# Optimization experiments

Hardware: AMD Instinct MI355X
Metric: run time of the kernel (lower is better)

Reference implementation:

```python
import jax, jax.numpy as jnp
import numpy as np

N, E, D, H, G, OUT = 50000, 800000, 128, 128, 64, 10


def setup_inputs() -> dict:
    key = jax.random.key(0)
    ks = jax.random.split(key, 10)
    x = jax.random.normal(ks[0], (N, D), dtype=jnp.float32)
    edge_index = jax.random.randint(ks[1], (2, E), 0, N, dtype=jnp.int64)
    batch = jnp.sort(jax.random.randint(ks[2], (N,), 0, G, dtype=jnp.int64))
    s = 1.0 / np.sqrt(D)
    W0 = jax.random.normal(ks[3], (D, H), dtype=jnp.float32) * s
    W1 = jax.random.normal(ks[4], (H, H), dtype=jnp.float32) * s
    W2 = jax.random.normal(ks[5], (H, H), dtype=jnp.float32) * s
    M0w = jax.random.normal(ks[6], (H, H), dtype=jnp.float32) * s
    M0b = jnp.zeros((H,), dtype=jnp.float32)
    M1w = jax.random.normal(ks[7], (H, OUT), dtype=jnp.float32) * s
    M1b = jnp.zeros((OUT,), dtype=jnp.float32)
    return dict(x=x, W0=W0, W1=W1, W2=W2, M0w=M0w, M0b=M0b, M1w=M1w, M1b=M1b,
                edge_index=edge_index, batch=batch)


def gcn_conv(x, W, src, dst):
    # PyG GCNConv (bias=False): h = x @ W; out = D^-1/2 (A + I) D^-1/2 h
    h = x @ W
    deg = jnp.zeros((N,), h.dtype).at[dst].add(1.0) + 1.0  # +1 for self-loop
    dinv = deg ** -0.5
    w = dinv[src] * dinv[dst]  # [E]
    agg = jax.ops.segment_sum(h[src] * w[:, None], dst, num_segments=N)
    return agg + h * (dinv * dinv)[:, None]  # self-loop term


def reference(x, W0, W1, W2, M0w, M0b, M1w, M1b, edge_index, batch):
    src, dst = edge_index[0], edge_index[1]
    h = gcn_conv(x, W0, src, dst)
    h = gcn_conv(jax.nn.relu(h), W1, src, dst)
    h = gcn_conv(jax.nn.relu(h), W2, src, dst)
    # global mean pool over graphs
    sums = jax.ops.segment_sum(h, batch, num_segments=G)
    cnts = jax.ops.segment_sum(jnp.ones((N,), h.dtype), batch, num_segments=G)
    pooled = sums / jnp.maximum(cnts, 1.0)[:, None]
    out = pooled @ M0w + M0b
    out = jax.nn.relu(out) @ M1w + M1b
    return out
```

## Files before the change

### kernel.cpp

```cpp
#include <hip/hip_runtime.h>
#include <hip/hip_fp16.h>

#define NN 50000
#define NE 800000
#define DIM 128
#define NG 64
#define NOUT 10

#define NBKT 391
#define HBLK 256
#define CHUNK ((NE + HBLK - 1) / HBLK)
#define PSLICE 8

typedef __attribute__((ext_vector_type(8))) short short8;
typedef __attribute__((ext_vector_type(4))) float float4v;

__device__ __forceinline__ void bf16_split(float v, short& hi, short& lo) {
    unsigned u = __float_as_uint(v);
    unsigned hb = (u + 0x7FFFu + ((u >> 16) & 1u)) & 0xFFFF0000u;
    float res = v - __uint_as_float(hb);
    unsigned u2 = __float_as_uint(res);
    unsigned lb = (u2 + 0x7FFFu + ((u2 >> 16) & 1u)) >> 16;
    hi = (short)(hb >> 16);
    lo = (short)lb;
}

#define PREP_XB 48
#define PREP_HB (PREP_XB + NN * DIM / 2048)
#define PREP_NB (PREP_HB + HBLK + 1)
__global__ __launch_bounds__(256) void prep_kernel(const float* __restrict__ W0,
                                                   const float* __restrict__ W1,
                                                   const float* __restrict__ W2,
                                                   short* __restrict__ wsp,
                                                   const float* __restrict__ X,
                                                   short* __restrict__ Ahi,
                                                   short* __restrict__ Alo,
                                                   const int* __restrict__ ei,
                                                   int* __restrict__ blkhist,
                                                   const int* __restrict__ batch,
                                                   int* __restrict__ first) {
    __shared__ int h[NBKT];
    int bx = blockIdx.x;
    if (bx < PREP_XB) {
        int w = bx >> 4;
        int sub = bx & 15;
        const float* W = (w == 0) ? W0 : (w == 1) ? W1 : W2;
        short* Wh = wsp + w * 2 * DIM * DIM;
        short* Wl = Wh + DIM * DIM;
        #pragma unroll
        for (int t = 0; t < 4; ++t) {
            int idx = sub * 1024 + t * 256 + threadIdx.x;
            int k = idx >> 7, n = idx & 127;
            short hi, lo;
            bf16_split(W[idx], hi, lo);
            Wh[n * DIM + k] = hi;
            Wl[n * DIM + k] = lo;
        }
    } else if (bx < PREP_HB) {
        size_t base = (size_t)(bx - PREP_XB) * 2048;
        #pragma unroll
        for (int c = 0; c < 2; ++c) {
            size_t idx = base + c * 1024 + threadIdx.x * 4;
            float4 v = *(const float4*)(X + idx);
            short h0, l0, h1, l1, h2, l2, h3, l3;
            bf16_split(v.x, h0, l0);
            bf16_split(v.y, h1, l1);
            bf16_split(v.z, h2, l2);
            bf16_split(v.w, h3, l3);
            *(ushort4*)(Ahi + idx) = make_ushort4((unsigned short)h0, (unsigned short)h1,
                                                  (unsigned short)h2, (unsigned short)h3);
            *(ushort4*)(Alo + idx) = make_ushort4((unsigned short)l0, (unsigned short)l1,
                                                  (unsigned short)l2, (unsigned short)l3);
        }
    } else if (bx < PREP_NB - 1) {
        int b = bx - PREP_HB;
        for (int i = threadIdx.x; i < NBKT; i += 256) h[i] = 0;
        __syncthreads();
        int lo = b * CHUNK, hi = min(lo + CHUNK, NE);
        for (int e = lo + threadIdx.x; e < hi; e += 256)
            atomicAdd(&h[ei[NE + e] >> 7], 1);
        __syncthreads();
        for (int i = threadIdx.x; i < NBKT; i += 256)
            blkhist[b * NBKT + i] = h[i];
    } else {
        int g = threadIdx.x;
        if (g <= NG) {
            int lo = 0, hi = NN;
            while (lo < hi) {
                int mid = (lo + hi) >> 1;
                if (batch[mid] < g) lo = mid + 1; else hi = mid;
            }
            first[g] = lo;
        }
    }
}

__global__ __launch_bounds__(256) void scan_all(int* __restrict__ blkhist,
                                                int* __restrict__ bintot) {
    __shared__ int s[256];
    int bin = blockIdx.x;
    int t = threadIdx.x;
    int v = blkhist[t * NBKT + bin];
    s[t] = v;
    __syncthreads();
    #pragma unroll
    for (int off = 1; off < 256; off <<= 1) {
        int tv = (t >= off) ? s[t - off] : 0;
        __syncthreads();
        s[t] += tv;
        __syncthreads();
    }
    blkhist[t * NBKT + bin] = s[t] - v;
    if (t == 255) bintot[bin] = s[255];
}

__global__ __launch_bounds__(512) void base_scan_kernel(const int* __restrict__ bintot,
                                                        int* __restrict__ bucket_base) {
    __shared__ int s[512];
    int t = threadIdx.x;
    int v = (t < NBKT) ? bintot[t] : 0;
    s[t] = v;
    __syncthreads();
    #pragma unroll
    for (int off = 1; off < 512; off <<= 1) {
        int tv = (t >= off) ? s[t - off] : 0;
        __syncthreads();
        s[t] += tv;
        __syncthreads();
    }
    if (t <= NBKT) bucket_base[t] = s[t] - v;
}

__global__ __launch_bounds__(256) void bucket_scatter(const int* __restrict__ ei,
                                                      const int* __restrict__ blkhist,
                                                      const int* __restrict__ bucket_base,
                                                      unsigned* __restrict__ ebuf) {
    __shared__ int cur[NBKT];
    int b = blockIdx.x;
    for (int i = threadIdx.x; i < NBKT; i += 256)
        cur[i] = blkhist[b * NBKT + i] + bucket_base[i];
    __syncthreads();
    int lo = b * CHUNK, hi = min(lo + CHUNK, NE);
    for (int e = lo + threadIdx.x; e < hi; e += 256) {
        int s = ei[e];
        int d = ei[NE + e];
        int pos = atomicAdd(&cur[d >> 7], 1);
        ebuf[pos] = ((unsigned)(d & 127) << 16) | (unsigned)s;
    }
}

__global__ __launch_bounds__(128) void build_csr(const unsigned* __restrict__ ebuf,
                                                 const int* __restrict__ bucket_base,
                                                 int* __restrict__ rowoff,
                                                 int* __restrict__ csr_src,
                                                 float* __restrict__ dinv) {
    __shared__ int deg[128];
    __shared__ int loff[128];
    int g = blockIdx.x;
    int lo = bucket_base[g], hi = bucket_base[g + 1];
    int t = threadIdx.x;
    deg[t] = 0;
    __syncthreads();
    for (int p = lo + t; p < hi; p += 128)
        atomicAdd(&deg[ebuf[p] >> 16], 1);
    __syncthreads();
    int v = deg[t];
    loff[t] = v;
    __syncthreads();
    #pragma unroll
    for (int off = 1; off < 128; off <<= 1) {
        int tv = (t >= off) ? loff[t - off] : 0;
        __syncthreads();
        loff[t] += tv;
        __syncthreads();
    }
    int excl = loff[t] - v;
    int node = g * 128 + t;
    if (node < NN) {
        rowoff[node] = lo + excl;
        dinv[node] = 1.0f / sqrtf((float)v + 1.0f);
    }
    if (node == 0) rowoff[NN] = NE;
    deg[t] = lo + excl;
    __syncthreads();
    for (int p = lo + t; p < hi; p += 128) {
        unsigned pk = ebuf[p];
        int pos = atomicAdd(&deg[pk >> 16], 1);
        csr_src[pos] = (int)(pk & 0xFFFFu);
    }
}

#define WPAD 136
__global__ __launch_bounds__(256) void gemm_mfma(const short* __restrict__ Ahi,
                                                 const short* __restrict__ Alo,
                                                 const short* __restrict__ Wsp,
                                                 __half* __restrict__ Y, int nrows) {
    __shared__ short Wh[DIM * WPAD];
    __shared__ short Wl[DIM * WPAD];
    int tid = threadIdx.x;
    {
        const short8* gh = (const short8*)Wsp;
        const short8* gl = (const short8*)(Wsp + DIM * DIM);
        #pragma unroll
        for (int i = 0; i < 8; ++i) {
            int e = tid + 256 * i;
            int n = e >> 4;
            int k = (e & 15) * 8;
            *(short8*)&Wh[n * WPAD + k] = gh[e];
            *(short8*)&Wl[n * WPAD + k] = gl[e];
        }
    }
    int wave = tid >> 6;
    int lane = tid & 63;
    int lm = lane & 15;
    int lq = lane >> 4;
    int row_t0 = blockIdx.x * 128 + wave * 32;

    float4v acc[2][8];
    #pragma unroll
    for (int t = 0; t < 2; ++t)
        #pragma unroll
        for (int i = 0; i < 8; ++i) acc[t][i] = (float4v){0.f, 0.f, 0.f, 0.f};

    __syncthreads();
    #pragma unroll
    for (int kk = 0; kk < 4; ++kk) {
        short8 ah[2], al[2];
        #pragma unroll
        for (int t = 0; t < 2; ++t) {
            int r = min(row_t0 + t * 16 + lm, nrows - 1);
            size_t ao = (size_t)r * DIM + kk * 32 + lq * 8;
            ah[t] = *(const short8*)(Ahi + ao);
            al[t] = *(const short8*)(Alo + ao);
        }
        #pragma unroll
        for (int n0 = 0; n0 < 8; ++n0) {
            short8 bh = *(const short8*)&Wh[(n0 * 16 + lm) * WPAD + kk * 32 + lq * 8];
            short8 bl = *(const short8*)&Wl[(n0 * 16 + lm) * WPAD + kk * 32 + lq * 8];
            #pragma unroll
            for (int t = 0; t < 2; ++t) {
                acc[t][n0] = __builtin_amdgcn_mfma_f32_16x16x32_bf16(ah[t], bh, acc[t][n0], 0, 0, 0);
                acc[t][n0] = __builtin_amdgcn_mfma_f32_16x16x32_bf16(al[t], bh, acc[t][n0], 0, 0, 0);
                acc[t][n0] = __builtin_amdgcn_mfma_f32_16x16x32_bf16(ah[t], bl, acc[t][n0], 0, 0, 0);
            }
        }
    }
    #pragma unroll
    for (int t = 0; t < 2; ++t)
        #pragma unroll
        for (int n0 = 0; n0 < 8; ++n0)
            #pragma unroll
            for (int rg = 0; rg < 4; ++rg) {
                int row = row_t0 + t * 16 + lq * 4 + rg;
                if (row < nrows) Y[(size_t)row * DIM + n0 * 16 + lm] = __float2half(acc[t][n0][rg]);
            }
}

template <bool SPLIT>
__global__ __launch_bounds__(128) void agg_kernel(const __half* __restrict__ H,
                                                  __half* __restrict__ O16,
                                                  short* __restrict__ Ohi,
                                                  short* __restrict__ Olo,
                                                  const int* __restrict__ rowoff,
                                                  const int* __restrict__ csr_src,
                                                  const float* __restrict__ dinv) {
    __shared__ float part[8][DIM];
    int i = blockIdx.x;
    int tid = threadIdx.x;
    int grp = tid >> 4;
    int ln = tid & 15;
    int s = rowoff[i], e = rowoff[i + 1];
    const __half* Hc = H + ln * 8;

    float a[8] = {0.f, 0.f, 0.f, 0.f, 0.f, 0.f, 0.f, 0.f};
    int p = s + grp;
    for (; p + 8 < e; p += 16) {
        int u0 = csr_src[p];
        int u1 = csr_src[p + 8];
        float d0 = dinv[u0], d1 = dinv[u1];
        short8 q0 = *(const short8*)(Hc + (size_t)u0 * DIM);
        short8 q1 = *(const short8*)(Hc + (size_t)u1 * DIM);
        #pragma unroll
        for (int k = 0; k < 8; ++k) {
            a[k] = fmaf(d0, __half2float(((const __half*)&q0)[k]), a[k]);
            a[k] = fmaf(d1, __half2float(((const __half*)&q1)[k]), a[k]);
        }
    }
    if (p < e) {
        int u = csr_src[p];
        float d = dinv[u];
        short8 q = *(const short8*)(Hc + (size_t)u * DIM);
        #pragma unroll
        for (int k = 0; k < 8; ++k)
            a[k] = fmaf(d, __half2float(((const __half*)&q)[k]), a[k]);
    }
    #pragma unroll
    for (int k = 0; k < 8; k += 4)
        *(float4*)&part[grp][ln * 8 + k] = make_float4(a[k], a[k + 1], a[k + 2], a[k + 3]);
    __syncthreads();
    int col = tid;
    float tot = 0.f;
    #pragma unroll
    for (int g2 = 0; g2 < 8; ++g2) tot += part[g2][col];
    float di = dinv[i];
    tot = fmaf(di, __half2float(H[(size_t)i * DIM + col]), tot);
    float v = di * tot;
    if (SPLIT) {
        v = fmaxf(v, 0.0f);
        short hi, lo;
        bf16_split(v, hi, lo);
        Ohi[(size_t)i * DIM + col] = hi;
        Olo[(size_t)i * DIM + col] = lo;
    } else {
        O16[(size_t)i * DIM + col] = __float2half(v);
    }
}

union U4 { ushort4 u; __half h[4]; };
__global__ __launch_bounds__(128) void pool_part(const __half* __restrict__ H,
                                                 const int* __restrict__ first,
                                                 float* __restrict__ ppart) {
    __shared__ float part[4][DIM];
    int g = blockIdx.x;
    int sl = blockIdx.y;
    int tid = threadIdx.x;
    int rg = tid >> 5, ln = tid & 31;
    int s = first[g], e = first[g + 1];
    float a0 = 0.f, a1 = 0.f, a2 = 0.f, a3 = 0.f;
    for (int r = s + sl * 4 + rg; r < e; r += PSLICE * 4) {
        U4 w;
        w.u = *(const ushort4*)(H + (size_t)r * DIM + ln * 4);
        a0 += __half2float(w.h[0]);
        a1 += __half2float(w.h[1]);
        a2 += __half2float(w.h[2]);
        a3 += __half2float(w.h[3]);
    }
    *(float4*)&part[rg][ln * 4] = make_float4(a0, a1, a2, a3);
    __syncthreads();
    float tot = part[0][tid] + part[1][tid] + part[2][tid] + part[3][tid];
    ppart[(size_t)(g * PSLICE + sl) * DIM + tid] = tot;
}

__global__ __launch_bounds__(128) void mlp_kernel(const float* __restrict__ ppart,
                                                  const int* __restrict__ first,
                                                  const float* __restrict__ M0w,
                                                  const float* __restrict__ M0b,
                                                  const float* __restrict__ M1w,
                                                  const float* __restrict__ M1b,
                                                  float* __restrict__ out) {
    __shared__ float p[DIM];
    __shared__ float t[DIM];
    int g = blockIdx.x;
    int j = threadIdx.x;
    float tot = 0.f;
    #pragma unroll
    for (int sl = 0; sl < PSLICE; ++sl)
        tot += ppart[(size_t)(g * PSLICE + sl) * DIM + j];
    float cnt = (float)max(first[g + 1] - first[g], 1);
    p[j] = tot / cnt;
    __syncthreads();
    float acc = M0b[j];
    #pragma unroll 8
    for (int k = 0; k < DIM; ++k) acc = fmaf(p[k], M0w[k * DIM + j], acc);
    t[j] = fmaxf(acc, 0.0f);
    __syncthreads();
    if (j < NOUT) {
        float o = M1b[j];
        #pragma unroll 8
        for (int k = 0; k < DIM; ++k) o = fmaf(t[k], M1w[k * NOUT + j], o);
        out[g * NOUT + j] = o;
    }
}

extern "C" void kernel_launch(void* const* d_in, const int* in_sizes, int n_in,
                              void* d_out, int out_size, void* d_ws, size_t ws_size,
                              hipStream_t stream) {
    const float* x   = (const float*)d_in[0];
    const float* W0  = (const float*)d_in[1];
    const float* W1  = (const float*)d_in[2];
    const float* W2  = (const float*)d_in[3];
    const float* M0w = (const float*)d_in[4];
    const float* M0b = (const float*)d_in[5];
    const float* M1w = (const float*)d_in[6];
    const float* M1b = (const float*)d_in[7];
    const int* ei    = (const int*)d_in[8];
    const int* batch = (const int*)d_in[9];
    float* out = (float*)d_out;

    char* ws = (char*)d_ws;
    size_t off = 0;
    auto take = [&](size_t bytes) -> void* {
        void* p = ws + off;
        off = (off + bytes + 255) & ~(size_t)255;
        return p;
    };
    __half* hA   = (__half*)take((size_t)NN * DIM * 2);
    __half* hB   = (__half*)take((size_t)NN * DIM * 2);
    short* Ahi   = (short*)take((size_t)NN * DIM * 2);
    short* Alo   = (short*)take((size_t)NN * DIM * 2);
    unsigned* ebuf = (unsigned*)take((size_t)NE * 4);
    int* csr_src = (int*)take((size_t)NE * 4);
    int* blkhist = (int*)take((size_t)HBLK * NBKT * 4);
    int* bintot  = (int*)take((size_t)NBKT * 4);
    int* bucket_base = (int*)take((size_t)(NBKT + 1) * 4);
    int* rowoff  = (int*)take((size_t)(NN + 1) * 4);
    float* dinv  = (float*)take((size_t)NN * 4);
    int* first   = (int*)take((size_t)(NG + 1) * 4);
    float* ppart = (float*)take((size_t)NG * PSLICE * DIM * 4);
    short* wsp   = (short*)take((size_t)3 * 2 * DIM * DIM * 2);
    (void)ws_size; (void)in_sizes; (void)n_in; (void)out_size;

    prep_kernel<<<PREP_NB, 256, 0, stream>>>(W0, W1, W2, wsp, x, Ahi, Alo,
                                             ei, blkhist, batch, first);
    scan_all<<<NBKT, 256, 0, stream>>>(blkhist, bintot);
    base_scan_kernel<<<1, 512, 0, stream>>>(bintot, bucket_base);
    bucket_scatter<<<HBLK, 256, 0, stream>>>(ei, blkhist, bucket_base, ebuf);
    build_csr<<<NBKT, 128, 0, stream>>>(ebuf, bucket_base, rowoff, csr_src, dinv);

    const int GB = (NN + 127) / 128;
    gemm_mfma<<<GB, 256, 0, stream>>>(Ahi, Alo, wsp, hA, NN);
    agg_kernel<true><<<NN, 128, 0, stream>>>(hA, nullptr, Ahi, Alo, rowoff, csr_src, dinv);
    gemm_mfma<<<GB, 256, 0, stream>>>(Ahi, Alo, wsp + 2 * DIM * DIM, hA, NN);
    agg_kernel<true><<<NN, 128, 0, stream>>>(hA, nullptr, Ahi, Alo, rowoff, csr_src, dinv);
    gemm_mfma<<<GB, 256, 0, stream>>>(Ahi, Alo, wsp + 4 * DIM * DIM, hA, NN);
    agg_kernel<false><<<NN, 128, 0, stream>>>(hA, hB, nullptr, nullptr, rowoff, csr_src, dinv);

    dim3 pgrid(NG, PSLICE);
    pool_part<<<pgrid, 128, 0, stream>>>(hB, first, ppart);
    mlp_kernel<<<NG, 128, 0, stream>>>(ppart, first, M0w, M0b, M1w, M1b, out);
}
```

Baseline: 284.3 us.

## Switch GEMM from bf16 three-pass split to fp16 two-pass with fp16 activations

Result: faster. 278.7 us (-2.0%).

```diff
diff --git a/kernel.cpp b/kernel.cpp
--- a/kernel.cpp
+++ b/kernel.cpp
@@ -13,35 +13,34 @@
 #define PSLICE 8
 
 typedef __attribute__((ext_vector_type(8))) short short8;
+typedef __attribute__((ext_vector_type(8))) _Float16 half8;
 typedef __attribute__((ext_vector_type(4))) float float4v;
 
-__device__ __forceinline__ void bf16_split(float v, short& hi, short& lo) {
-    unsigned u = __float_as_uint(v);
-    unsigned hb = (u + 0x7FFFu + ((u >> 16) & 1u)) & 0xFFFF0000u;
-    float res = v - __uint_as_float(hb);
-    unsigned u2 = __float_as_uint(res);
-    unsigned lb = (u2 + 0x7FFFu + ((u2 >> 16) & 1u)) >> 16;
-    hi = (short)(hb >> 16);
-    lo = (short)lb;
-}
-
-#define PREP_XB 48
-#define PREP_HB (PREP_XB + NN * DIM / 2048)
-#define PREP_NB (PREP_HB + HBLK + 1)
+union S8H8 { short8 s; half8 h; };
+union SH { short s; _Float16 h; };
+
+__device__ __forceinline__ void f16_split(float v, short& hi, short& lo) {
+    SH a, b;
+    a.h = (_Float16)v;
+    b.h = (_Float16)(v - (float)a.h);
+    hi = a.s;
+    lo = b.s;
+}
+
+#define PREP_WB 48
+#define PREP_HB (PREP_WB + HBLK)
+#define PREP_NB (PREP_HB + 1)
 __global__ __launch_bounds__(256) void prep_kernel(const float* __restrict__ W0,
                                                    const float* __restrict__ W1,
                                                    const float* __restrict__ W2,
                                                    short* __restrict__ wsp,
-                                                   const float* __restrict__ X,
-                                                   short* __restrict__ Ahi,
-                                                   short* __restrict__ Alo,
                                                    const int* __restrict__ ei,
                                                    int* __restrict__ blkhist,
                                                    const int* __restrict__ batch,
                                                    int* __restrict__ first) {
     __shared__ int h[NBKT];
     int bx = blockIdx.x;
-    if (bx < PREP_XB) {
+    if (bx < PREP_WB) {
         int w = bx >> 4;
         int sub = bx & 15;
         const float* W = (w == 0) ? W0 : (w == 1) ? W1 : W2;
@@ -52,28 +51,12 @@
             int idx = sub * 1024 + t * 256 + threadIdx.x;
             int k = idx >> 7, n = idx & 127;
             short hi, lo;
-            bf16_split(W[idx], hi, lo);
+            f16_split(W[idx], hi, lo);
             Wh[n * DIM + k] = hi;
             Wl[n * DIM + k] = lo;
         }
     } else if (bx < PREP_HB) {
-        size_t base = (size_t)(bx - PREP_XB) * 2048;
-        #pragma unroll
-        for (int c = 0; c < 2; ++c) {
-            size_t idx = base + c * 1024 + threadIdx.x * 4;
-            float4 v = *(const float4*)(X + idx);
-            short h0, l0, h1, l1, h2, l2, h3, l3;
-            bf16_split(v.x, h0, l0);
-            bf16_split(v.y, h1, l1);
-            bf16_split(v.z, h2, l2);
-            bf16_split(v.w, h3, l3);
-            *(ushort4*)(Ahi + idx) = make_ushort4((unsigned short)h0, (unsigned short)h1,
-                                                  (unsigned short)h2, (unsigned short)h3);
-            *(ushort4*)(Alo + idx) = make_ushort4((unsigned short)l0, (unsigned short)l1,
-                                                  (unsigned short)l2, (unsigned short)l3);
-        }
-    } else if (bx < PREP_NB - 1) {
-        int b = bx - PREP_HB;
+        int b = bx - PREP_WB;
         for (int i = threadIdx.x; i < NBKT; i += 256) h[i] = 0;
         __syncthreads();
         int lo = b * CHUNK, hi = min(lo + CHUNK, NE);
@@ -191,8 +174,9 @@
 }
 
 #define WPAD 136
-__global__ __launch_bounds__(256) void gemm_mfma(const short* __restrict__ Ahi,
-                                                 const short* __restrict__ Alo,
+template <bool AF32>
+__global__ __launch_bounds__(256) void gemm_mfma(const float* __restrict__ Xf,
+                                                 const __half* __restrict__ Xh,
                                                  const short* __restrict__ Wsp,
                                                  __half* __restrict__ Y, int nrows) {
     __shared__ short Wh[DIM * WPAD];
@@ -225,23 +209,33 @@
     __syncthreads();
     #pragma unroll
     for (int kk = 0; kk < 4; ++kk) {
-        short8 ah[2], al[2];
+        half8 a[2];
         #pragma unroll
         for (int t = 0; t < 2; ++t) {
             int r = min(row_t0 + t * 16 + lm, nrows - 1);
             size_t ao = (size_t)r * DIM + kk * 32 + lq * 8;
-            ah[t] = *(const short8*)(Ahi + ao);
-            al[t] = *(const short8*)(Alo + ao);
+            if (AF32) {
+                float4 xa = *(const float4*)(Xf + ao);
+                float4 xb = *(const float4*)(Xf + ao + 4);
+                a[t][0] = (_Float16)xa.x; a[t][1] = (_Float16)xa.y;
+                a[t][2] = (_Float16)xa.z; a[t][3] = (_Float16)xa.w;
+                a[t][4] = (_Float16)xb.x; a[t][5] = (_Float16)xb.y;
+                a[t][6] = (_Float16)xb.z; a[t][7] = (_Float16)xb.w;
+            } else {
+                S8H8 u;
+                u.s = *(const short8*)((const short*)Xh + ao);
+                a[t] = u.h;
+            }
         }
         #pragma unroll
         for (int n0 = 0; n0 < 8; ++n0) {
-            short8 bh = *(const short8*)&Wh[(n0 * 16 + lm) * WPAD + kk * 32 + lq * 8];
-            short8 bl = *(const short8*)&Wl[(n0 * 16 + lm) * WPAD + kk * 32 + lq * 8];
+            S8H8 bh, bl;
+            bh.s = *(const short8*)&Wh[(n0 * 16 + lm) * WPAD + kk * 32 + lq * 8];
+            bl.s = *(const short8*)&Wl[(n0 * 16 + lm) * WPAD + kk * 32 + lq * 8];
             #pragma unroll
             for (int t = 0; t < 2; ++t) {
-                acc[t][n0] = __builtin_amdgcn_mfma_f32_16x16x32_bf16(ah[t], bh, acc[t][n0], 0, 0, 0);
-                acc[t][n0] = __builtin_amdgcn_mfma_f32_16x16x32_bf16(al[t], bh, acc[t][n0], 0, 0, 0);
-                acc[t][n0] = __builtin_amdgcn_mfma_f32_16x16x32_bf16(ah[t], bl, acc[t][n0], 0, 0, 0);
+                acc[t][n0] = __builtin_amdgcn_mfma_f32_16x16x32_f16(a[t], bh.h, acc[t][n0], 0, 0, 0);
+                acc[t][n0] = __builtin_amdgcn_mfma_f32_16x16x32_f16(a[t], bl.h, acc[t][n0], 0, 0, 0);
             }
         }
     }
@@ -256,11 +250,9 @@
             }
 }
 
-template <bool SPLIT>
+template <bool RELU>
 __global__ __launch_bounds__(128) void agg_kernel(const __half* __restrict__ H,
                                                   __half* __restrict__ O16,
-                                                  short* __restrict__ Ohi,
-                                                  short* __restrict__ Olo,
                                                   const int* __restrict__ rowoff,
                                                   const int* __restrict__ csr_src,
                                                   const float* __restrict__ dinv) {
@@ -305,15 +297,8 @@
     float di = dinv[i];
     tot = fmaf(di, __half2float(H[(size_t)i * DIM + col]), tot);
     float v = di * tot;
-    if (SPLIT) {
-        v = fmaxf(v, 0.0f);
-        short hi, lo;
-        bf16_split(v, hi, lo);
-        Ohi[(size_t)i * DIM + col] = hi;
-        Olo[(size_t)i * DIM + col] = lo;
-    } else {
-        O16[(size_t)i * DIM + col] = __float2half(v);
-    }
+    if (RELU) v = fmaxf(v, 0.0f);
+    O16[(size_t)i * DIM + col] = __float2half(v);
 }
 
 union U4 { ushort4 u; __half h[4]; };
@@ -396,8 +381,6 @@
     };
     __half* hA   = (__half*)take((size_t)NN * DIM * 2);
     __half* hB   = (__half*)take((size_t)NN * DIM * 2);
-    short* Ahi   = (short*)take((size_t)NN * DIM * 2);
-    short* Alo   = (short*)take((size_t)NN * DIM * 2);
     unsigned* ebuf = (unsigned*)take((size_t)NE * 4);
     int* csr_src = (int*)take((size_t)NE * 4);
     int* blkhist = (int*)take((size_t)HBLK * NBKT * 4);
@@ -410,20 +393,19 @@
     short* wsp   = (short*)take((size_t)3 * 2 * DIM * DIM * 2);
     (void)ws_size; (void)in_sizes; (void)n_in; (void)out_size;
 
-    prep_kernel<<<PREP_NB, 256, 0, stream>>>(W0, W1, W2, wsp, x, Ahi, Alo,
-                                             ei, blkhist, batch, first);
+    prep_kernel<<<PREP_NB, 256, 0, stream>>>(W0, W1, W2, wsp, ei, blkhist, batch, first);
     scan_all<<<NBKT, 256, 0, stream>>>(blkhist, bintot);
     base_scan_kernel<<<1, 512, 0, stream>>>(bintot, bucket_base);
     bucket_scatter<<<HBLK, 256, 0, stream>>>(ei, blkhist, bucket_base, ebuf);
     build_csr<<<NBKT, 128, 0, stream>>>(ebuf, bucket_base, rowoff, csr_src, dinv);
 
     const int GB = (NN + 127) / 128;
-    gemm_mfma<<<GB, 256, 0, stream>>>(Ahi, Alo, wsp, hA, NN);
-    agg_kernel<true><<<NN, 128, 0, stream>>>(hA, nullptr, Ahi, Alo, rowoff, csr_src, dinv);
-    gemm_mfma<<<GB, 256, 0, stream>>>(Ahi, Alo, wsp + 2 * DIM * DIM, hA, NN);
-    agg_kernel<true><<<NN, 128, 0, stream>>>(hA, nullptr, Ahi, Alo, rowoff, csr_src, dinv);
-    gemm_mfma<<<GB, 256, 0, stream>>>(Ahi, Alo, wsp + 4 * DIM * DIM, hA, NN);
-    agg_kernel<false><<<NN, 128, 0, stream>>>(hA, hB, nullptr, nullptr, rowoff, csr_src, dinv);
+    gemm_mfma<true><<<GB, 256, 0, stream>>>(x, nullptr, wsp, hA, NN);
+    agg_kernel<true><<<NN, 128, 0, stream>>>(hA, hB, rowoff, csr_src, dinv);
+    gemm_mfma<false><<<GB, 256, 0, stream>>>(nullptr, hB, wsp + 2 * DIM * DIM, hA, NN);
+    agg_kernel<true><<<NN, 128, 0, stream>>>(hA, hB, rowoff, csr_src, dinv);
+    gemm_mfma<false><<<GB, 256, 0, stream>>>(nullptr, hB, wsp + 4 * DIM * DIM, hA, NN);
+    agg_kernel<false><<<NN, 128, 0, stream>>>(hA, hB, rowoff, csr_src, dinv);
 
     dim3 pgrid(NG, PSLICE);
     pool_part<<<pgrid, 128, 0, stream>>>(hB, first, ppart);
```
